# Performance work log

Measured on AMD Instinct MI355X. Metric: run time of the kernel, lower is better.

The kernel has to match this reference:

```python
import jax, jax.numpy as jnp
import numpy as np

B, T, D, U = 32, 2048, 512, 512

def setup_inputs() -> dict:
    key = jax.random.key(0)
    ks = jax.random.split(key, 8)
    s = 0.02
    return {
        "query": jax.random.normal(ks[0], (B, D), dtype=jnp.float32),
        "values": jax.random.normal(ks[1], (B, T, D), dtype=jnp.float32),
        "W1_w": jax.random.normal(ks[2], (D, U), dtype=jnp.float32) * s,
        "W1_b": jnp.zeros((U,), dtype=jnp.float32),
        "W2_w": jax.random.normal(ks[3], (D, U), dtype=jnp.float32) * s,
        "W2_b": jnp.zeros((U,), dtype=jnp.float32),
        "V_w": jax.random.normal(ks[4], (U, 1), dtype=jnp.float32) * s,
        "V_b": jnp.zeros((1,), dtype=jnp.float32),
    }

def reference(query, values, W1_w, W1_b, W2_w, W2_b, V_w, V_b):
    # query: [B, D] -> [B, 1, U]; values: [B, T, D] -> [B, T, U]
    q_proj = (query @ W1_w + W1_b)[:, None, :]              # [B, 1, U]
    v_proj = jnp.einsum('btd,du->btu', values, W2_w) + W2_b  # [B, T, U]
    score = jnp.tanh(q_proj + v_proj) @ V_w + V_b            # [B, T, 1]
    attn = jax.nn.softmax(score, axis=1)                     # [B, T, 1]
    context = jnp.sum(attn * values, axis=1)                 # [B, D]
    return context, attn
```

## Files before the change

kernel.cpp:

```cpp
#include <hip/hip_runtime.h>
#include <hip/hip_bf16.h>
#include <cstddef>

#define B_ 32
#define T_ 2048
#define D_ 512
#define U_ 512

typedef __attribute__((ext_vector_type(8))) short bf16x8;
typedef __attribute__((ext_vector_type(4))) float f32x4;

__device__ __forceinline__ unsigned short f2bf(float f) {
  union { float f; unsigned u; } x; x.f = f;
  unsigned r = x.u + 0x7fffu + ((x.u >> 16) & 1u);
  return (unsigned short)(r >> 16);
}
__device__ __forceinline__ unsigned pack2bf(float a, float b) {
  return (unsigned)f2bf(a) | ((unsigned)f2bf(b) << 16);
}
__device__ __forceinline__ float tanh_fast(float x) {
  float e = __expf(2.0f * x);
  return 1.0f - 2.0f * __builtin_amdgcn_rcpf(e + 1.0f);
}

__global__ void kA_prep(const float* __restrict__ W2, unsigned* __restrict__ W2P,
                        const float* __restrict__ query, const float* __restrict__ W1,
                        const float* __restrict__ W1b, const float* __restrict__ W2b,
                        float* __restrict__ qp, float* __restrict__ score,
                        float* __restrict__ ctx) {
  const int tid = threadIdx.x;
  if (blockIdx.x < 256) {
    #pragma unroll
    for (int ii = 0; ii < 2; ++ii) {
      int p = blockIdx.x * 512 + ii * 256 + tid;
      int j = (p & 3) * 2;
      int l = (p >> 2) & 63;
      int t = p >> 8;
      int u = (t >> 4) * 16 + (l & 15);
      int k = (t & 15) * 32 + ((l >> 4) << 3) + j;
      W2P[p] = pack2bf(W2[(size_t)k * U_ + u], W2[(size_t)(k + 1) * U_ + u]);
    }
  } else {
    __shared__ float qs[D_];
    const int blk = blockIdx.x - 256;
    const int b = blk >> 1, uhh = (blk & 1) * 256;
    qs[tid] = query[b * D_ + tid];
    qs[tid + 256] = query[b * D_ + tid + 256];
    __syncthreads();
    const int u = uhh + tid;
    float a0 = 0, a1 = 0, a2 = 0, a3 = 0, a4 = 0, a5 = 0, a6 = 0, a7 = 0;
    for (int d = 0; d < D_; d += 8) {
      a0 += qs[d + 0] * W1[(size_t)(d + 0) * U_ + u];
      a1 += qs[d + 1] * W1[(size_t)(d + 1) * U_ + u];
      a2 += qs[d + 2] * W1[(size_t)(d + 2) * U_ + u];
      a3 += qs[d + 3] * W1[(size_t)(d + 3) * U_ + u];
      a4 += qs[d + 4] * W1[(size_t)(d + 4) * U_ + u];
      a5 += qs[d + 5] * W1[(size_t)(d + 5) * U_ + u];
      a6 += qs[d + 6] * W1[(size_t)(d + 6) * U_ + u];
      a7 += qs[d + 7] * W1[(size_t)(d + 7) * U_ + u];
    }
    qp[b * U_ + u] = ((a0 + a1) + (a2 + a3)) + ((a4 + a5) + (a6 + a7)) + W1b[u] + W2b[u];
    const int gt = blk * 256 + tid;
    ctx[gt] = 0.0f;
    #pragma unroll
    for (int i = 0; i < 4; ++i) score[i * 16384 + gt] = 0.0f;
  }
}

__global__ __launch_bounds__(256, 3) void k2_score(
    const float* __restrict__ values, const unsigned short* __restrict__ W2P,
    const float* __restrict__ qp, const float* __restrict__ Vw,
    float* __restrict__ score) {
  constexpr int LS = 264;
  __shared__ unsigned short av[64 * LS];
  __shared__ float qv[256];
  __shared__ float vwv[256];
  const int tid = threadIdx.x;
  const int bx = blockIdx.x;
  const int mt = bx >> 1, uh = bx & 1;
  const int m0 = mt * 64;
  const int b = m0 >> 11;
  const int ub = uh * 256;
  qv[tid] = qp[b * U_ + ub + tid];
  vwv[tid] = Vw[ub + tid];

  const int l = tid & 63, w = tid >> 6;
  const int lr = l & 15, lq = l >> 4;

  f32x4 acc[4][4];
  #pragma unroll
  for (int mi = 0; mi < 4; ++mi)
    #pragma unroll
    for (int ni = 0; ni < 4; ++ni) acc[mi][ni] = (f32x4){0.f, 0.f, 0.f, 0.f};

  const unsigned short* bw = W2P + (size_t)(uh * 16 + w * 4) * 8192 + (size_t)l * 8;
  const int abase = lr * LS + lq * 8;

  #pragma unroll
  for (int half = 0; half < 2; ++half) {
    const float4* vb = (const float4*)(values + (size_t)m0 * D_ + half * 256);
    #pragma unroll
    for (int it = 0; it < 16; ++it) {
      int i = tid + it * 256;
      int row = i >> 6, c4 = i & 63;
      float4 v = vb[(size_t)row * 128 + c4];
      uint2 p; p.x = pack2bf(v.x, v.y); p.y = pack2bf(v.z, v.w);
      *(uint2*)&av[row * LS + c4 * 4] = p;
    }
    __syncthreads();
    const int kg0 = half * 8;
    bf16x8 b0[4], b1[4];
    #pragma unroll
    for (int ni = 0; ni < 4; ++ni)
      b0[ni] = *(const bf16x8*)(bw + (size_t)ni * 8192 + (size_t)kg0 * 512);
    #pragma unroll
    for (int kk = 0; kk < 8; ++kk) {
      bf16x8* cur = (kk & 1) ? b1 : b0;
      bf16x8* nxt = (kk & 1) ? b0 : b1;
      if (kk < 7) {
        #pragma unroll
        for (int ni = 0; ni < 4; ++ni)
          nxt[ni] = *(const bf16x8*)(bw + (size_t)ni * 8192 + (size_t)(kg0 + kk + 1) * 512);
      }
      bf16x8 a[4];
      #pragma unroll
      for (int mi = 0; mi < 4; ++mi)
        a[mi] = *(const bf16x8*)&av[abase + mi * 16 * LS + kk * 32];
      #pragma unroll
      for (int ni = 0; ni < 4; ++ni)
        #pragma unroll
        for (int mi = 0; mi < 4; ++mi)
          acc[mi][ni] = __builtin_amdgcn_mfma_f32_16x16x32_bf16(a[mi], cur[ni], acc[mi][ni], 0, 0, 0);
    }
    __syncthreads();
  }

  float sacc[4][4];
  #pragma unroll
  for (int mi = 0; mi < 4; ++mi)
    #pragma unroll
    for (int r = 0; r < 4; ++r) sacc[mi][r] = 0.0f;
  #pragma unroll
  for (int ni = 0; ni < 4; ++ni) {
    int ul = w * 64 + ni * 16 + lr;
    float qpv = qv[ul], vv = vwv[ul];
    #pragma unroll
    for (int mi = 0; mi < 4; ++mi)
      #pragma unroll
      for (int r = 0; r < 4; ++r)
        sacc[mi][r] += tanh_fast(acc[mi][ni][r] + qpv) * vv;
  }
  #pragma unroll
  for (int mi = 0; mi < 4; ++mi)
    #pragma unroll
    for (int r = 0; r < 4; ++r) {
      float v = sacc[mi][r];
      v += __shfl_xor(v, 1); v += __shfl_xor(v, 2);
      v += __shfl_xor(v, 4); v += __shfl_xor(v, 8);
      if (lr == 0) atomicAdd(&score[m0 + mi * 16 + lq * 4 + r], v);
    }
}

__global__ void k3_softmax(const float* __restrict__ score, float* __restrict__ attn) {
  __shared__ float red[8];
  const int b = blockIdx.x, tid = threadIdx.x;
  const float* s = score + b * T_;
  float v[8];
  float mx = -1e30f;
  #pragma unroll
  for (int i = 0; i < 8; ++i) { v[i] = s[tid + i * 256]; mx = fmaxf(mx, v[i]); }
  #pragma unroll
  for (int off = 1; off < 64; off <<= 1) mx = fmaxf(mx, __shfl_xor(mx, off));
  if ((tid & 63) == 0) red[tid >> 6] = mx;
  __syncthreads();
  mx = fmaxf(fmaxf(red[0], red[1]), fmaxf(red[2], red[3]));
  float sum = 0.0f;
  #pragma unroll
  for (int i = 0; i < 8; ++i) { v[i] = __expf(v[i] - mx); sum += v[i]; }
  #pragma unroll
  for (int off = 1; off < 64; off <<= 1) sum += __shfl_xor(sum, off);
  if ((tid & 63) == 0) red[4 + (tid >> 6)] = sum;
  __syncthreads();
  sum = (red[4] + red[5]) + (red[6] + red[7]);
  float inv = 1.0f / sum;
  #pragma unroll
  for (int i = 0; i < 8; ++i) attn[b * T_ + tid + i * 256] = v[i] * inv;
}

__global__ void k4_ctx(const float* __restrict__ values, const float* __restrict__ attn,
                       float* __restrict__ ctx) {
  __shared__ float at[64];
  __shared__ float ps[512];
  const int blk = blockIdx.x;
  const int b = blk >> 5, tc = blk & 31;
  const int tid = threadIdx.x;
  if (tid < 64) at[tid] = attn[b * T_ + tc * 64 + tid];
  __syncthreads();
  const int q = tid & 127;
  const int r0 = tid >> 7;
  const float4* vb = (const float4*)(values + ((size_t)b * T_ + tc * 64) * D_);
  float ax = 0.f, ay = 0.f, az = 0.f, aw = 0.f;
  #pragma unroll 8
  for (int tt = 0; tt < 32; ++tt) {
    int row = tt * 2 + r0;
    float4 v = vb[(size_t)row * 128 + q];
    float a = at[row];
    ax += a * v.x; ay += a * v.y; az += a * v.z; aw += a * v.w;
  }
  if (r0 == 1) { ps[4 * q] = ax; ps[4 * q + 1] = ay; ps[4 * q + 2] = az; ps[4 * q + 3] = aw; }
  __syncthreads();
  if (r0 == 0) {
    atomicAdd(&ctx[b * D_ + 4 * q + 0], ax + ps[4 * q + 0]);
    atomicAdd(&ctx[b * D_ + 4 * q + 1], ay + ps[4 * q + 1]);
    atomicAdd(&ctx[b * D_ + 4 * q + 2], az + ps[4 * q + 2]);
    atomicAdd(&ctx[b * D_ + 4 * q + 3], aw + ps[4 * q + 3]);
  }
}

extern "C" void kernel_launch(void* const* d_in, const int* in_sizes, int n_in,
                              void* d_out, int out_size, void* d_ws, size_t ws_size,
                              hipStream_t stream) {
  const float* query = (const float*)d_in[0];
  const float* values = (const float*)d_in[1];
  const float* W1w = (const float*)d_in[2];
  const float* W1b = (const float*)d_in[3];
  const float* W2w = (const float*)d_in[4];
  const float* W2b = (const float*)d_in[5];
  const float* Vw  = (const float*)d_in[6];

  float* out = (float*)d_out;
  float* ctx  = out;
  float* attn = out + B_ * D_;
  float* score = attn;

  char* ws = (char*)d_ws;
  unsigned* W2P = (unsigned*)ws;
  float* qp    = (float*)(ws + 512 * 1024);

  kA_prep<<<320, 256, 0, stream>>>(W2w, W2P, query, W1w, W1b, W2b, qp, score, ctx);
  k2_score<<<2048, 256, 0, stream>>>(values, (const unsigned short*)W2P, qp, Vw, score);
  k3_softmax<<<32, 256, 0, stream>>>(score, attn);
  k4_ctx<<<1024, 256, 0, stream>>>(values, attn, ctx);
}
```

Measured before the change: 296.8 us.

## Pre-pack values into MFMA-fragment bf16 layout and stream GEMM operands from global

Adds a separate pack kernel that converts values to bf16 in the exact MFMA fragment order, then a score kernel that loads both A and B operands directly from global memory with register double/triple buffering instead of staging through LDS. This is meant to remove the LDS staging, the syncthreads and the in-loop conversion from the score GEMM. In exchange it adds a full extra pass that writes 64MB of packed values, and it needs a large workspace; the old path is kept as a fallback when the workspace is too small.

```diff
diff --git a/kernel.cpp b/kernel.cpp
--- a/kernel.cpp
+++ b/kernel.cpp
@@ -67,7 +67,115 @@
   }
 }
 
-__global__ __launch_bounds__(256, 3) void k2_score(
+__global__ void kB_pack(const float* __restrict__ values, unsigned* __restrict__ VP) {
+  constexpr int LS = 260;
+  __shared__ float st[32 * LS];
+  const int mb = blockIdx.x;
+  const int tid = threadIdx.x;
+  #pragma unroll
+  for (int half = 0; half < 2; ++half) {
+    const float* vsrc = values + (size_t)mb * 32 * D_ + half * 256;
+    #pragma unroll
+    for (int it = 0; it < 8; ++it) {
+      int i = tid + it * 256;
+      int row = i >> 6, c4 = i & 63;
+      float4 v = *(const float4*)(vsrc + (size_t)row * D_ + c4 * 4);
+      *(float4*)&st[row * LS + c4 * 4] = v;
+    }
+    __syncthreads();
+    #pragma unroll
+    for (int n = 0; n < 16; ++n) {
+      int q = tid + n * 256;
+      int tm = q >> 11;
+      int kgl = (q >> 8) & 7;
+      int lo = (q >> 2) & 63;
+      int jp = q & 3;
+      int mloc = tm * 16 + (lo & 15);
+      int kloc = kgl * 32 + ((lo >> 4) << 3) + jp * 2;
+      unsigned pk = pack2bf(st[mloc * LS + kloc], st[mloc * LS + kloc + 1]);
+      VP[(size_t)((mb * 2 + tm) * 16 + half * 8 + kgl) * 256 + lo * 4 + jp] = pk;
+    }
+    __syncthreads();
+  }
+}
+
+__global__ __launch_bounds__(256, 3) void k2_stream(
+    const unsigned short* __restrict__ VP, const unsigned short* __restrict__ W2P,
+    const float* __restrict__ qp, const float* __restrict__ Vw,
+    float* __restrict__ score) {
+  const int tid = threadIdx.x;
+  const int bx = blockIdx.x;
+  const int mbk = bx >> 1, uh = bx & 1;
+  const int m0 = mbk * 64;
+  const int b = m0 >> 11;
+  const int l = tid & 63, w = tid >> 6;
+  const int lr = l & 15, lq = l >> 4;
+
+  f32x4 acc[4][4];
+  #pragma unroll
+  for (int mi = 0; mi < 4; ++mi)
+    #pragma unroll
+    for (int ni = 0; ni < 4; ++ni) acc[mi][ni] = (f32x4){0.f, 0.f, 0.f, 0.f};
+
+  const unsigned short* Ab = VP + (size_t)(mbk * 4) * 8192 + (size_t)l * 8;
+  const unsigned short* Bb = W2P + (size_t)(uh * 16 + w * 4) * 8192 + (size_t)l * 8;
+
+  bf16x8 Ar[3][4], Br[2][4];
+  #pragma unroll
+  for (int mi = 0; mi < 4; ++mi) Ar[0][mi] = *(const bf16x8*)(Ab + (size_t)mi * 8192);
+  #pragma unroll
+  for (int ni = 0; ni < 4; ++ni) Br[0][ni] = *(const bf16x8*)(Bb + (size_t)ni * 8192);
+  #pragma unroll
+  for (int mi = 0; mi < 4; ++mi) Ar[1][mi] = *(const bf16x8*)(Ab + (size_t)mi * 8192 + 512);
+
+  #pragma unroll
+  for (int kg = 0; kg < 16; ++kg) {
+    const int ca = kg % 3, cb = kg & 1;
+    if (kg < 14) {
+      const int na = (kg + 2) % 3;
+      #pragma unroll
+      for (int mi = 0; mi < 4; ++mi)
+        Ar[na][mi] = *(const bf16x8*)(Ab + (size_t)mi * 8192 + (size_t)(kg + 2) * 512);
+    }
+    if (kg < 15) {
+      #pragma unroll
+      for (int ni = 0; ni < 4; ++ni)
+        Br[cb ^ 1][ni] = *(const bf16x8*)(Bb + (size_t)ni * 8192 + (size_t)(kg + 1) * 512);
+    }
+    #pragma unroll
+    for (int ni = 0; ni < 4; ++ni)
+      #pragma unroll
+      for (int mi = 0; mi < 4; ++mi)
+        acc[mi][ni] = __builtin_amdgcn_mfma_f32_16x16x32_bf16(Ar[ca][mi], Br[cb][ni], acc[mi][ni], 0, 0, 0);
+  }
+
+  float sacc[4][4];
+  #pragma unroll
+  for (int mi = 0; mi < 4; ++mi)
+    #pragma unroll
+    for (int r = 0; r < 4; ++r) sacc[mi][r] = 0.0f;
+  #pragma unroll
+  for (int ni = 0; ni < 4; ++ni) {
+    int u = uh * 256 + w * 64 + ni * 16 + lr;
+    float qpv = qp[b * U_ + u], vv = Vw[u];
+    #pragma unroll
+    for (int mi = 0; mi < 4; ++mi)
+      #pragma unroll
+      for (int r = 0; r < 4; ++r)
+        sacc[mi][r] += tanh_fast(acc[mi][ni][r] + qpv) * vv;
+  }
+  #pragma unroll
+  for (int mi = 0; mi < 4; ++mi)
+    #pragma unroll
+    for (int r = 0; r < 4; ++r) {
+      float v = sacc[mi][r];
+      v += __shfl_xor(v, 1); v += __shfl_xor(v, 2);
+      v += __shfl_xor(v, 4); v += __shfl_xor(v, 8);
+      if (lr == 0) atomicAdd(&score[m0 + mi * 16 + lq * 4 + r], v);
+    }
+}
+
+__global__ __launch_bounds__(256, 3) void k2_score_lds(
     const float* __restrict__ values, const unsigned short* __restrict__ W2P,
     const float* __restrict__ qp, const float* __restrict__ Vw,
     float* __restrict__ score) {
@@ -83,19 +191,15 @@
   const int ub = uh * 256;
   qv[tid] = qp[b * U_ + ub + tid];
   vwv[tid] = Vw[ub + tid];
-
   const int l = tid & 63, w = tid >> 6;
   const int lr = l & 15, lq = l >> 4;
-
   f32x4 acc[4][4];
   #pragma unroll
   for (int mi = 0; mi < 4; ++mi)
     #pragma unroll
     for (int ni = 0; ni < 4; ++ni) acc[mi][ni] = (f32x4){0.f, 0.f, 0.f, 0.f};
-
   const unsigned short* bw = W2P + (size_t)(uh * 16 + w * 4) * 8192 + (size_t)l * 8;
   const int abase = lr * LS + lq * 8;
-
   #pragma unroll
   for (int half = 0; half < 2; ++half) {
     const float4* vb = (const float4*)(values + (size_t)m0 * D_ + half * 256);
@@ -134,7 +238,6 @@
     }
     __syncthreads();
   }
-
   float sacc[4][4];
   #pragma unroll
   for (int mi = 0; mi < 4; ++mi)
@@ -236,9 +339,18 @@
   char* ws = (char*)d_ws;
   unsigned* W2P = (unsigned*)ws;
   float* qp    = (float*)(ws + 512 * 1024);
+  unsigned* VP  = (unsigned*)(ws + 576 * 1024);
+  const size_t VP_BYTES = (size_t)B_ * T_ * D_ * 2;
+  const bool big_ws = ws_size >= 576 * 1024 + VP_BYTES;
 
   kA_prep<<<320, 256, 0, stream>>>(W2w, W2P, query, W1w, W1b, W2b, qp, score, ctx);
-  k2_score<<<2048, 256, 0, stream>>>(values, (const unsigned short*)W2P, qp, Vw, score);
+  if (big_ws) {
+    kB_pack<<<2048, 256, 0, stream>>>(values, VP);
+    k2_stream<<<2048, 256, 0, stream>>>((const unsigned short*)VP, (const unsigned short*)W2P,
+                                        qp, Vw, score);
+  } else {
+    k2_score_lds<<<2048, 256, 0, stream>>>(values, (const unsigned short*)W2P, qp, Vw, score);
+  }
   k3_softmax<<<32, 256, 0, stream>>>(score, attn);
   k4_ctx<<<1024, 256, 0, stream>>>(values, attn, ctx);
 }
```

Result: slower. 316.2 us (+6.5%).

## Stream values into LDS via global_load_lds with double-buffered K pipeline

Applied to the files above, without the earlier changes.

The score kernel now copies fp32 values tiles directly into shared memory with asynchronous global_load_lds, double-buffered across eight K chunks of 64. The bf16 conversion moves to after the LDS read, using a cheaper round-half-up perm-based pack. W2 fragments are prefetched one stage ahead. The aim is to overlap global loads with MFMA work and drop the register round trip. In exchange the fp32 staging doubles LDS bytes per element, occupancy drops from 3 to 2 blocks, there are more barriers, and the rounding changes slightly (ties round up rather than to even).

```diff
diff --git a/kernel.cpp b/kernel.cpp
--- a/kernel.cpp
+++ b/kernel.cpp
@@ -1,6 +1,7 @@
 #include <hip/hip_runtime.h>
 #include <hip/hip_bf16.h>
 #include <cstddef>
+#include <cstdint>
 
 #define B_ 32
 #define T_ 2048
@@ -18,10 +19,17 @@
 __device__ __forceinline__ unsigned pack2bf(float a, float b) {
   return (unsigned)f2bf(a) | ((unsigned)f2bf(b) << 16);
 }
+__device__ __forceinline__ unsigned pack2bf_fast(float a, float b) {
+  union { float f; unsigned u; } xa, xb; xa.f = a; xb.f = b;
+  return __builtin_amdgcn_perm(xb.u + 0x8000u, xa.u + 0x8000u, 0x07060302u);
+}
 __device__ __forceinline__ float tanh_fast(float x) {
   float e = __expf(2.0f * x);
   return 1.0f - 2.0f * __builtin_amdgcn_rcpf(e + 1.0f);
 }
+
+#define AS1C(p) ((const __attribute__((address_space(1))) unsigned*)(p))
+#define AS3(p)  ((__attribute__((address_space(3))) unsigned*)(p))
 
 __global__ void kA_prep(const float* __restrict__ W2, unsigned* __restrict__ W2P,
                         const float* __restrict__ query, const float* __restrict__ W1,
@@ -67,72 +75,82 @@
   }
 }
 
-__global__ __launch_bounds__(256, 3) void k2_score(
+__global__ __launch_bounds__(256, 2) void k2_dma(
     const float* __restrict__ values, const unsigned short* __restrict__ W2P,
     const float* __restrict__ qp, const float* __restrict__ Vw,
     float* __restrict__ score) {
-  constexpr int LS = 264;
-  __shared__ unsigned short av[64 * LS];
-  __shared__ float qv[256];
-  __shared__ float vwv[256];
+  constexpr int GS = 260;
+  __shared__ float av[2][16 * GS];
   const int tid = threadIdx.x;
   const int bx = blockIdx.x;
   const int mt = bx >> 1, uh = bx & 1;
   const int m0 = mt * 64;
   const int b = m0 >> 11;
-  const int ub = uh * 256;
-  qv[tid] = qp[b * U_ + ub + tid];
-  vwv[tid] = Vw[ub + tid];
-
   const int l = tid & 63, w = tid >> 6;
   const int lr = l & 15, lq = l >> 4;
 
+  const int drow = l >> 4;
+  const int dcol = (l & 15) * 4;
+
   f32x4 acc[4][4];
   #pragma unroll
   for (int mi = 0; mi < 4; ++mi)
     #pragma unroll
     for (int ni = 0; ni < 4; ++ni) acc[mi][ni] = (f32x4){0.f, 0.f, 0.f, 0.f};
 
-  const unsigned short* bw = W2P + (size_t)(uh * 16 + w * 4) * 8192 + (size_t)l * 8;
-  const int abase = lr * LS + lq * 8;
-
-  #pragma unroll
-  for (int half = 0; half < 2; ++half) {
-    const float4* vb = (const float4*)(values + (size_t)m0 * D_ + half * 256);
-    #pragma unroll
-    for (int it = 0; it < 16; ++it) {
-      int i = tid + it * 256;
-      int row = i >> 6, c4 = i & 63;
-      float4 v = vb[(size_t)row * 128 + c4];
-      uint2 p; p.x = pack2bf(v.x, v.y); p.y = pack2bf(v.z, v.w);
-      *(uint2*)&av[row * LS + c4 * 4] = p;
-    }
+  const unsigned short* Bb = W2P + (size_t)(uh * 16 + w * 4) * 8192 + (size_t)l * 8;
+
+  auto stage = [&](int e, int p) {
+    #pragma unroll
+    for (int j = 0; j < 4; ++j) {
+      int g = w * 4 + j;
+      const float* gp = values + (size_t)(m0 + g * 4 + drow) * D_ + e * 64 + dcol;
+      __builtin_amdgcn_global_load_lds(AS1C(gp), AS3(&av[p][g * GS]), 16, 0, 0);
+    }
+  };
+
+  bf16x8 Bf[2][2][4];
+  stage(0, 0);
+  #pragma unroll
+  for (int kq = 0; kq < 2; ++kq)
+    #pragma unroll
+    for (int ni = 0; ni < 4; ++ni)
+      Bf[0][kq][ni] = *(const bf16x8*)(Bb + (size_t)ni * 8192 + (size_t)kq * 512);
+
+  const int afb = (lr >> 2) * GS + (lr & 3) * 64 + lq * 8;
+
+  for (int e = 0; e < 8; ++e) {
+    const int p = e & 1;
     __syncthreads();
-    const int kg0 = half * 8;
-    bf16x8 b0[4], b1[4];
-    #pragma unroll
-    for (int ni = 0; ni < 4; ++ni)
-      b0[ni] = *(const bf16x8*)(bw + (size_t)ni * 8192 + (size_t)kg0 * 512);
-    #pragma unroll
-    for (int kk = 0; kk < 8; ++kk) {
-      bf16x8* cur = (kk & 1) ? b1 : b0;
-      bf16x8* nxt = (kk & 1) ? b0 : b1;
-      if (kk < 7) {
+    if (e < 7) {
+      stage(e + 1, p ^ 1);
+      #pragma unroll
+      for (int kq = 0; kq < 2; ++kq)
         #pragma unroll
         for (int ni = 0; ni < 4; ++ni)
-          nxt[ni] = *(const bf16x8*)(bw + (size_t)ni * 8192 + (size_t)(kg0 + kk + 1) * 512);
+          Bf[p ^ 1][kq][ni] = *(const bf16x8*)(Bb + (size_t)ni * 8192 + (size_t)(2 * e + 2 + kq) * 512);
+    }
+    #pragma unroll
+    for (int kq = 0; kq < 2; ++kq) {
+      bf16x8 a[4];
+      #pragma unroll
+      for (int mi = 0; mi < 4; ++mi) {
+        const float* ap = &av[p][mi * 4 * GS + afb + kq * 32];
+        f32x4 f0 = *(const f32x4*)ap;
+        f32x4 f1 = *(const f32x4*)(ap + 4);
+        unsigned u0 = pack2bf_fast(f0.x, f0.y);
+        unsigned u1 = pack2bf_fast(f0.z, f0.w);
+        unsigned u2 = pack2bf_fast(f1.x, f1.y);
+        unsigned u3 = pack2bf_fast(f1.z, f1.w);
+        unsigned au[4] = {u0, u1, u2, u3};
+        a[mi] = *(const bf16x8*)au;
       }
-      bf16x8 a[4];
-      #pragma unroll
-      for (int mi = 0; mi < 4; ++mi)
-        a[mi] = *(const bf16x8*)&av[abase + mi * 16 * LS + kk * 32];
       #pragma unroll
       for (int ni = 0; ni < 4; ++ni)
         #pragma unroll
         for (int mi = 0; mi < 4; ++mi)
-          acc[mi][ni] = __builtin_amdgcn_mfma_f32_16x16x32_bf16(a[mi], cur[ni], acc[mi][ni], 0, 0, 0);
-    }
-    __syncthreads();
+          acc[mi][ni] = __builtin_amdgcn_mfma_f32_16x16x32_bf16(a[mi], Bf[p][kq][ni], acc[mi][ni], 0, 0, 0);
+    }
   }
 
   float sacc[4][4];
@@ -142,8 +160,8 @@
     for (int r = 0; r < 4; ++r) sacc[mi][r] = 0.0f;
   #pragma unroll
   for (int ni = 0; ni < 4; ++ni) {
-    int ul = w * 64 + ni * 16 + lr;
-    float qpv = qv[ul], vv = vwv[ul];
+    int u = uh * 256 + w * 64 + ni * 16 + lr;
+    float qpv = qp[b * U_ + u], vv = Vw[u];
     #pragma unroll
     for (int mi = 0; mi < 4; ++mi)
       #pragma unroll
@@ -238,7 +256,7 @@
   float* qp    = (float*)(ws + 512 * 1024);
 
   kA_prep<<<320, 256, 0, stream>>>(W2w, W2P, query, W1w, W1b, W2b, qp, score, ctx);
-  k2_score<<<2048, 256, 0, stream>>>(values, (const unsigned short*)W2P, qp, Vw, score);
+  k2_dma<<<2048, 256, 0, stream>>>(values, (const unsigned short*)W2P, qp, Vw, score);
   k3_softmax<<<32, 256, 0, stream>>>(score, attn);
   k4_ctx<<<1024, 256, 0, stream>>>(values, attn, ctx);
 }
```

Result: faster. 287.1 us (-3.3%).
